# Kernel tuning notes

Hardware: AMD Instinct MI355X
Metric: run time of the kernel (lower is better)

## Reference

```python
import jax, jax.numpy as jnp
import numpy as np

# ---- static config (matches init_kwargs) ----
B, N, D, FH, FW, C = 2, 6, 48, 16, 44, 80
OGH, OGW, DOWNSAMPLE = 256, 704, 16
D_MIN, D_MAX = 2.0, 58.0
XB = (-51.2, 51.2, 0.4); YB = (-51.2, 51.2, 0.4); ZB = (-10.0, 10.0, 20.0)
NX, NY, NZ = 256, 256, 1  # (ub-lb)/step per bound
DX = jnp.array([XB[2], YB[2], ZB[2]], jnp.float32)
LOWER = jnp.array([XB[0], YB[0], ZB[0]], jnp.float32)  # bx - dx/2


def _frustum():
    # UD depth discretization: d_i = d_min + i*(d_max-d_min)/D
    ds = D_MIN + (D_MAX - D_MIN) / D * np.arange(D, dtype=np.float32)
    ds = np.broadcast_to(ds[:, None, None], (D, FH, FW))
    xs = np.broadcast_to(np.linspace(0, OGW - 1, FW, dtype=np.float32)[None, None, :], (D, FH, FW))
    ys = np.broadcast_to(np.linspace(0, OGH - 1, FH, dtype=np.float32)[None, :, None], (D, FH, FW))
    return jnp.asarray(np.stack([xs, ys, ds], -1))  # [D,FH,FW,3]

FRUSTUM = _frustum()


def setup_inputs() -> dict:
    key = jax.random.key(0)
    k1, k2 = jax.random.split(key)
    x = jax.random.normal(k1, (B, N, D, FH, FW, C), dtype=jnp.float32)
    # camera-to-ego rotation: ego_x = z_cam (fwd), ego_y = -x_cam, ego_z = -y_cam
    R = np.array([[0.0, 0.0, 1.0], [-1.0, 0.0, 0.0], [0.0, -1.0, 0.0]], np.float32)
    rots = jnp.asarray(np.broadcast_to(R, (B, N, 3, 3)).copy())
    trans = 2.0 * jax.random.normal(k2, (B, N, 3), dtype=jnp.float32)
    K = np.array([[500.0, 0.0, OGW / 2.0], [0.0, 500.0, OGH / 2.0], [0.0, 0.0, 1.0]], np.float32)
    intrins = jnp.asarray(np.broadcast_to(K, (B, N, 3, 3)).copy())
    post_rots = jnp.asarray(np.broadcast_to(np.eye(3, dtype=np.float32), (B, N, 3, 3)).copy())
    post_trans = jnp.zeros((B, N, 3), jnp.float32)
    return {"x": x, "rots": rots, "trans": trans, "intrins": intrins,
            "post_rots": post_rots, "post_trans": post_trans}


def _get_geometry(rots, trans, intrins, post_rots, post_trans):
    # frustum -> ego-frame 3D points: [B,N,D,FH,FW,3]
    pts = FRUSTUM[None, None] - post_trans[:, :, None, None, None, :]
    inv_post = jnp.linalg.inv(post_rots)
    pts = jnp.einsum('bnij,bndhwj->bndhwi', inv_post, pts)
    # un-normalize pixel coords by depth
    pts = jnp.concatenate([pts[..., :2] * pts[..., 2:3], pts[..., 2:3]], axis=-1)
    combine = jnp.einsum('bnij,bnjk->bnik', rots, jnp.linalg.inv(intrins))
    pts = jnp.einsum('bnij,bndhwj->bndhwi', combine, pts)
    return pts + trans[:, :, None, None, None, :]


def _voxel_pooling(geom, x):
    Nprime = B * N * D * FH * FW
    xf = x.reshape(Nprime, C)
    # voxel indices; torch .long() truncates toward zero -> astype matches
    gi = ((geom.reshape(Nprime, 3) - LOWER) / DX).astype(jnp.int32)
    batch_ix = jnp.repeat(jnp.arange(B, dtype=jnp.int32), Nprime // B)
    kept = ((gi[:, 0] >= 0) & (gi[:, 0] < NX) &
            (gi[:, 1] >= 0) & (gi[:, 1] < NY) &
            (gi[:, 2] >= 0) & (gi[:, 2] < NZ))
    gi = jnp.where(kept[:, None], gi, 0)
    # flat index into (B, NZ, NY, NX); equivalent aggregation to sort+quickcumsum
    flat = ((batch_ix * NZ + gi[:, 2]) * NY + gi[:, 1]) * NX + gi[:, 0]
    xm = jnp.where(kept[:, None], xf, 0.0)
    pooled = jax.ops.segment_sum(xm, flat, num_segments=B * NZ * NY * NX)
    final = pooled.reshape(B, NZ, NY, NX, C).transpose(0, 4, 1, 2, 3)
    return final  # [B, C, NZ, NY, NX]


def reference(x, rots, trans, intrins, post_rots, post_trans):
    geom = _get_geometry(rots, trans, intrins, post_rots, post_trans)
    return _voxel_pooling(geom, x)
```

## Files before the change

kernel.cpp:

```cpp
#include <hip/hip_runtime.h>


#define NCH       80
#define GRID_HW   65536
#define OUT_PER_B 5242880
#define HSTRIDE   3520
#define PTS_PER_BN 33792
#define CAP       32

#define N_ENT_MAX 405504
#define P_BYTES   129761280u
#define NEXT_OFF  129761280u
#define HEAD_OFF  131383296u
#define CNT_OFF   131907584u
#define META_OFF  131907840u
#define WS_NEED   133529856u

__device__ inline void inv3(const double a[9], double inv[9]) {
    double c00 =  a[4]*a[8] - a[5]*a[7];
    double c01 = -(a[3]*a[8] - a[5]*a[6]);
    double c02 =  a[3]*a[7] - a[4]*a[6];
    double det = a[0]*c00 + a[1]*c01 + a[2]*c02;
    double id  = 1.0/det;
    inv[0] = c00*id;
    inv[1] = (a[2]*a[7]-a[1]*a[8])*id;
    inv[2] = (a[1]*a[5]-a[2]*a[4])*id;
    inv[3] = c01*id;
    inv[4] = (a[0]*a[8]-a[2]*a[6])*id;
    inv[5] = (a[2]*a[3]-a[0]*a[5])*id;
    inv[6] = c02*id;
    inv[7] = (a[1]*a[6]-a[0]*a[7])*id;
    inv[8] = (a[0]*a[4]-a[1]*a[3])*id;
}

__device__ inline void prep_bn(const float* __restrict__ rots,
                               const float* __restrict__ trans,
                               const float* __restrict__ intrins,
                               const float* __restrict__ post_rots,
                               const float* __restrict__ post_trans,
                               int bn, double* o) {
    double pr[9], kk[9], rt[9], ipr[9], ik[9];
    #pragma unroll
    for (int i = 0; i < 9; i++) {
        pr[i] = (double)post_rots[bn*9 + i];
        kk[i] = (double)intrins[bn*9 + i];
        rt[i] = (double)rots[bn*9 + i];
    }
    inv3(pr, ipr);
    inv3(kk, ik);
    #pragma unroll
    for (int i = 0; i < 9; i++) o[i] = ipr[i];
    #pragma unroll
    for (int r = 0; r < 3; r++)
        #pragma unroll
        for (int c = 0; c < 3; c++)
            o[9 + r*3 + c] = rt[r*3+0]*ik[0*3+c] + rt[r*3+1]*ik[1*3+c] + rt[r*3+2]*ik[2*3+c];
    #pragma unroll
    for (int i = 0; i < 3; i++) o[18 + i] = (double)post_trans[bn*3 + i];
    #pragma unroll
    for (int i = 0; i < 3; i++) o[21 + i] = (double)trans[bn*3 + i];
}

__global__ void prep_kernel(const float* __restrict__ rots,
                            const float* __restrict__ trans,
                            const float* __restrict__ intrins,
                            const float* __restrict__ post_rots,
                            const float* __restrict__ post_trans,
                            double* __restrict__ tw) {
    int bn = threadIdx.x;
    if (bn >= 12) return;
    prep_bn(rots, trans, intrins, post_rots, post_trans, bn, tw + bn*24);
}

__global__ __launch_bounds__(256) void zero_kernel(float4* __restrict__ p, int n4) {
    int i = blockIdx.x * 256 + threadIdx.x;
    int stride = gridDim.x * 256;
    for (; i < n4; i += stride) p[i] = make_float4(0.f, 0.f, 0.f, 0.f);
}

__global__ __launch_bounds__(256) void init_heads(int* __restrict__ head, int* __restrict__ counter) {
    int i = blockIdx.x * 256 + threadIdx.x;
    if (i < 131072) head[i] = -1;
    if (i == 0) counter[0] = 0;
}

__device__ inline void geom_points(const double* __restrict__ t,
                                   int b, int d, int tid, int* s_base) {
    const float dsv = __fadd_rn(2.0f, __fmul_rn((float)(56.0 / 48.0), (float)d));
    for (int idx = tid; idx < 704; idx += 256) {
        const int h = idx / 44;
        const int w = idx - h * 44;
        float xsv = (w == 43) ? 703.0f : (float)((double)w * (703.0 / 43.0));
        float ysv = (float)(h * 17);
        double px = (double)xsv - t[18];
        double py = (double)ysv - t[19];
        double pz = (double)dsv - t[20];
        double q0 = t[0]*px + t[1]*py + t[2]*pz;
        double q1 = t[3]*px + t[4]*py + t[5]*pz;
        double q2 = t[6]*px + t[7]*py + t[8]*pz;
        q0 *= q2;
        q1 *= q2;
        double e0 = t[9]*q0  + t[10]*q1 + t[11]*q2 + t[21];
        double e1 = t[12]*q0 + t[13]*q1 + t[14]*q2 + t[22];
        double e2 = t[15]*q0 + t[16]*q1 + t[17]*q2 + t[23];
        const double lxy = (double)(-51.2f);
        const double dxy = (double)(0.4f);
        int gx = (int)((e0 - lxy) / dxy);
        int gy = (int)((e1 - lxy) / dxy);
        int gz = (int)((e2 - (double)(-10.0f)) / (double)(20.0f));
        int base = -1;
        if (gx >= 0 && gx < 256 && gy >= 0 && gy < 256 && gz == 0)
            base = (b << 16) | (gy << 8) | gx;
        s_base[idx] = base;
    }
}

__global__ __launch_bounds__(256) void geom_groups(const float* __restrict__ rots,
                                                   const float* __restrict__ trans,
                                                   const float* __restrict__ intrins,
                                                   const float* __restrict__ post_rots,
                                                   const float* __restrict__ post_trans,
                                                   int* __restrict__ nxt,
                                                   int* __restrict__ head,
                                                   int* __restrict__ counter,
                                                   unsigned* __restrict__ ent_meta) {
    __shared__ double   s_t[24];
    __shared__ int      s_base[704];
    __shared__ int      s_gbase[704];
    __shared__ unsigned s_gmask[704];
    __shared__ int      s_gcount[44];
    __shared__ int      s_goff[44];
    __shared__ int      s_eb;

    const int tid   = threadIdx.x;
    const int slice = blockIdx.x;
    const int bn    = slice / 48;
    const int d     = slice - bn * 48;
    const int b     = bn / 6;

    if (tid == 0)
        prep_bn(rots, trans, intrins, post_rots, post_trans, bn, s_t);
    __syncthreads();

    geom_points(s_t, b, d, tid, s_base);
    __syncthreads();

    if (tid < 44) {
        int gb[16]; unsigned gm[16];
        int cnt = 0;
        #pragma unroll
        for (int h = 0; h < 16; h++) {
            int pb = s_base[h * 44 + tid];
            if (pb >= 0) {
                int j = 0;
                for (; j < cnt; j++) if (gb[j] == pb) break;
                if (j < cnt) gm[j] |= (1u << h);
                else { gb[cnt] = pb; gm[cnt] = (1u << h); cnt++; }
            }
        }
        s_gcount[tid] = cnt;
        for (int j = 0; j < cnt; j++) {
            s_gbase[tid * 16 + j] = gb[j];
            s_gmask[tid * 16 + j] = gm[j];
        }
    }
    __syncthreads();

    if (tid == 0) {
        int off = 0;
        for (int w = 0; w < 44; w++) { s_goff[w] = off; off += s_gcount[w]; }
        s_eb = atomicAdd(counter, off);
    }
    __syncthreads();

    if (tid < 44) {
        int off = s_goff[tid];
        int cnt = s_gcount[tid];
        for (int k = 0; k < cnt; k++) {
            int e = s_eb + off + k;
            ent_meta[e] = ((unsigned)slice << 22) | ((unsigned)tid << 16)
                        | (s_gmask[tid * 16 + k] & 0xFFFFu);
            nxt[e] = atomicExch(&head[s_gbase[tid * 16 + k]], e);
        }
    }
}

__global__ __launch_bounds__(256) void reduce_kernel(const float* __restrict__ x,
                                                     const unsigned* __restrict__ ent_meta,
                                                     const int* __restrict__ counter,
                                                     float* __restrict__ P) {
    const int NE = counter[0];
    const int total = NE * 20;
    int i = blockIdx.x * 256 + threadIdx.x;
    const int stride = gridDim.x * 256;
    for (; i < total; i += stride) {
        int e  = i / 20;
        int c4 = i - e * 20;
        unsigned meta = ent_meta[e];
        int slice   = (int)(meta >> 22);
        int w       = (int)((meta >> 16) & 63u);
        unsigned mm = meta & 0xFFFFu;
        const float* xb = x + (size_t)(slice * 704 + w) * NCH + c4 * 4;
        float ax = 0.f, ay = 0.f, az = 0.f, aw = 0.f;
        #pragma unroll
        for (int h = 0; h < 16; h++) {
            float4 v = *(const float4*)(xb + h * HSTRIDE);
            float m = (float)((mm >> h) & 1u);
            ax = fmaf(m, v.x, ax);
            ay = fmaf(m, v.y, ay);
            az = fmaf(m, v.z, az);
            aw = fmaf(m, v.w, aw);
        }
        float4 r; r.x = ax; r.y = ay; r.z = az; r.w = aw;
        *(float4*)(P + (size_t)e * NCH + c4 * 4) = r;
    }
}

__global__ __launch_bounds__(256, 4) void gather_tiled(const float* __restrict__ P,
                                                       const int* __restrict__ nxt,
                                                       const int* __restrict__ head,
                                                       float* __restrict__ out) {
    __shared__ float tile[64 * 81];
    __shared__ int   s_ent[64 * CAP];
    __shared__ int   s_cnt[64];
    __shared__ int   s_ovf[64];

    const int tid = threadIdx.x;
    const int b   = blockIdx.x >> 10;
    const int v0  = (blockIdx.x & 1023) * 64;

    if (tid < 64) {
        int e = head[(b << 16) + v0 + tid];
        int c = 0;
        while (e >= 0 && c < CAP) { s_ent[tid * CAP + c] = e; c++; e = nxt[e]; }
        s_cnt[tid] = c;
        s_ovf[tid] = e;
    }
    __syncthreads();

    #pragma unroll
    for (int i = 0; i < 5; i++) {
        int j  = i * 256 + tid;
        int v  = j / 20;
        int c4 = j - v * 20;
        double dx = 0.0, dy = 0.0, dz = 0.0, dw = 0.0;
        const int cnt = s_cnt[v];
        for (int k = 0; k < cnt; k++) {
            const float4 p = *(const float4*)(P + (size_t)s_ent[v * CAP + k] * NCH + c4 * 4);
            dx += (double)p.x; dy += (double)p.y; dz += (double)p.z; dw += (double)p.w;
        }
        int e = s_ovf[v];
        while (e >= 0) {
            const float4 p = *(const float4*)(P + (size_t)e * NCH + c4 * 4);
            dx += (double)p.x; dy += (double)p.y; dz += (double)p.z; dw += (double)p.w;
            e = nxt[e];
        }
        tile[v * 81 + c4 * 4 + 0] = (float)dx;
        tile[v * 81 + c4 * 4 + 1] = (float)dy;
        tile[v * 81 + c4 * 4 + 2] = (float)dz;
        tile[v * 81 + c4 * 4 + 3] = (float)dw;
    }
    __syncthreads();

    float* dst = out + (size_t)b * OUT_PER_B + v0;
    #pragma unroll
    for (int i = 0; i < 20; i++) {
        int k  = i * 256 + tid;
        int c  = k >> 6;
        int lv = k & 63;
        dst[(size_t)c * GRID_HW + lv] = tile[lv * 81 + c];
    }
}

__global__ __launch_bounds__(256) void scatter_direct_kernel(const float* __restrict__ x,
                                                             const double* __restrict__ ws,
                                                             float* __restrict__ out) {
    __shared__ int      s_base[704];
    __shared__ int      s_colbase[44];
    __shared__ unsigned s_mask[44];
    __shared__ unsigned s_fb[44];

    const int tid = threadIdx.x;
    const int bn  = blockIdx.x / 48;
    const int d   = blockIdx.x - bn * 48;
    const int b   = bn / 6;
    geom_points(ws + bn * 24, b, d, tid, s_base);
    __syncthreads();

    if (tid < 44) {
        int cb = -1; unsigned mm = 0, fb = 0;
        #pragma unroll
        for (int h = 0; h < 16; h++) {
            int pb = s_base[h * 44 + tid];
            if (pb >= 0) {
                if (cb < 0) cb = pb;
                if (pb == cb) mm |= (1u << h);
                else          fb |= (1u << h);
            }
        }
        s_colbase[tid] = cb;
        s_mask[tid]    = mm;
        s_fb[tid]      = fb;
    }
    __syncthreads();

    const float* xb0 = x + ((size_t)bn * PTS_PER_BN + (size_t)d * 704) * NCH;
    #pragma unroll
    for (int pass = 0; pass < 4; pass++) {
        int item = pass * 256 + tid;
        if (item >= 880) break;
        int w  = item / 20;
        int c4 = item - w * 20;
        unsigned mm = s_mask[w];
        unsigned fb = s_fb[w];
        if (!(mm | fb)) continue;
        const float* xb = xb0 + (size_t)w * NCH + c4 * 4;
        float ax = 0.f, ay = 0.f, az = 0.f, aw = 0.f;
        #pragma unroll
        for (int h = 0; h < 16; h++) {
            if ((mm >> h) & 1u) {
                float4 v = *(const float4*)(xb + h * HSTRIDE);
                ax += v.x; ay += v.y; az += v.z; aw += v.w;
            } else if ((fb >> h) & 1u) {
                float4 v = *(const float4*)(xb + h * HSTRIDE);
                int vb = s_base[h * 44 + w];
                float* o = out + (size_t)(vb >> 16) * OUT_PER_B + (vb & 65535);
                atomicAdd(o + (size_t)(c4*4 + 0) * GRID_HW, v.x);
                atomicAdd(o + (size_t)(c4*4 + 1) * GRID_HW, v.y);
                atomicAdd(o + (size_t)(c4*4 + 2) * GRID_HW, v.z);
                atomicAdd(o + (size_t)(c4*4 + 3) * GRID_HW, v.w);
            }
        }
        if (mm) {
            int vb = s_colbase[w];
            float* o = out + (size_t)(vb >> 16) * OUT_PER_B + (vb & 65535);
            atomicAdd(o + (size_t)(c4*4 + 0) * GRID_HW, ax);
            atomicAdd(o + (size_t)(c4*4 + 1) * GRID_HW, ay);
            atomicAdd(o + (size_t)(c4*4 + 2) * GRID_HW, az);
            atomicAdd(o + (size_t)(c4*4 + 3) * GRID_HW, aw);
        }
    }
}

extern "C" void kernel_launch(void* const* d_in, const int* in_sizes, int n_in,
                              void* d_out, int out_size, void* d_ws, size_t ws_size,
                              hipStream_t stream) {
    const float* x          = (const float*)d_in[0];
    const float* rots       = (const float*)d_in[1];
    const float* trans      = (const float*)d_in[2];
    const float* intrins    = (const float*)d_in[3];
    const float* post_rots  = (const float*)d_in[4];
    const float* post_trans = (const float*)d_in[5];
    float* out = (float*)d_out;

    if (ws_size >= (size_t)WS_NEED) {
        float*    P       = (float*)d_ws;
        int*      nxt     = (int*)((char*)d_ws + NEXT_OFF);
        int*      head    = (int*)((char*)d_ws + HEAD_OFF);
        int*      counter = (int*)((char*)d_ws + CNT_OFF);
        unsigned* meta    = (unsigned*)((char*)d_ws + META_OFF);
        init_heads<<<512, 256, 0, stream>>>(head, counter);
        geom_groups<<<576, 256, 0, stream>>>(rots, trans, intrins,
                                             post_rots, post_trans,
                                             nxt, head, counter, meta);
        reduce_kernel<<<2048, 256, 0, stream>>>(x, meta, counter, P);
        gather_tiled<<<2048, 256, 0, stream>>>(P, nxt, head, out);
    } else if (ws_size >= 12 * 24 * sizeof(double)) {
        double* tw = (double*)d_ws;
        zero_kernel<<<2560, 256, 0, stream>>>((float4*)out, out_size / 16);
        prep_kernel<<<1, 64, 0, stream>>>(rots, trans, intrins, post_rots, post_trans, tw);
        scatter_direct_kernel<<<576, 256, 0, stream>>>(x, tw, out);
    }
}
```

Before: 229.9 us.

## Replace per-slice grouping with per-column geometry kernel using wave prefix-scan allocation

Replaces the block-per-slice geometry/grouping kernel with a kernel where each thread handles one image column: it computes 16 voxel ids and groups only consecutive equal voxels. Entry slots are allocated with a wavefront prefix scan and one atomic per wave. The gather switches from double to float accumulation and raises occupancy by halving CAP and allowing 6 blocks per CU. Init and reduce launch sizes also change. Non-adjacent duplicate voxels in a column now become separate entries, and float accumulation can slightly change rounding.

```diff
diff --git a/kernel.cpp b/kernel.cpp
--- a/kernel.cpp
+++ b/kernel.cpp
@@ -6,7 +6,8 @@
 #define OUT_PER_B 5242880
 #define HSTRIDE   3520
 #define PTS_PER_BN 33792
-#define CAP       32
+#define NCOLS     25344
+#define CAP       16
 
 #define N_ENT_MAX 405504
 #define P_BYTES   129761280u
@@ -78,10 +79,198 @@
     for (; i < n4; i += stride) p[i] = make_float4(0.f, 0.f, 0.f, 0.f);
 }
 
-__global__ __launch_bounds__(256) void init_heads(int* __restrict__ head, int* __restrict__ counter) {
+__global__ __launch_bounds__(256) void init_heads(int4* __restrict__ head4, int* __restrict__ counter) {
     int i = blockIdx.x * 256 + threadIdx.x;
-    if (i < 131072) head[i] = -1;
+    head4[i] = make_int4(-1, -1, -1, -1);
     if (i == 0) counter[0] = 0;
+}
+
+__global__ __launch_bounds__(256) void geom_cols(const float* __restrict__ rots,
+                                                 const float* __restrict__ trans,
+                                                 const float* __restrict__ intrins,
+                                                 const float* __restrict__ post_rots,
+                                                 const float* __restrict__ post_trans,
+                                                 int* __restrict__ nxt,
+                                                 int* __restrict__ head,
+                                                 int* __restrict__ counter,
+                                                 unsigned* __restrict__ ent_meta) {
+    __shared__ double s_t[12 * 24];
+
+    const int tid  = threadIdx.x;
+    const int col  = blockIdx.x * 256 + tid;
+    const int lane = tid & 63;
+
+    if (tid < 12)
+        prep_bn(rots, trans, intrins, post_rots, post_trans, tid, s_t + tid * 24);
+    __syncthreads();
+
+    const int slice = col / 44;
+    const int w     = col - slice * 44;
+    const int bn    = slice / 48;
+    const int d     = slice - bn * 48;
+    const int b     = bn / 6;
+    const double* t = s_t + bn * 24;
+
+    int vox[16];
+    {
+        const float dsv = __fadd_rn(2.0f, __fmul_rn((float)(56.0 / 48.0), (float)d));
+        const float xsv = (w == 43) ? 703.0f : (float)((double)w * (703.0 / 43.0));
+        const double px = (double)xsv - t[18];
+        #pragma unroll
+        for (int h = 0; h < 16; h++) {
+            float ysv = (float)(h * 17);
+            double py = (double)ysv - t[19];
+            double pz = (double)dsv - t[20];
+            double q0 = t[0]*px + t[1]*py + t[2]*pz;
+            double q1 = t[3]*px + t[4]*py + t[5]*pz;
+            double q2 = t[6]*px + t[7]*py + t[8]*pz;
+            q0 *= q2;
+            q1 *= q2;
+            double e0 = t[9]*q0  + t[10]*q1 + t[11]*q2 + t[21];
+            double e1 = t[12]*q0 + t[13]*q1 + t[14]*q2 + t[22];
+            double e2 = t[15]*q0 + t[16]*q1 + t[17]*q2 + t[23];
+            const double lxy = (double)(-51.2f);
+            const double dxy = (double)(0.4f);
+            int gx = (int)((e0 - lxy) / dxy);
+            int gy = (int)((e1 - lxy) / dxy);
+            int gz = (int)((e2 - (double)(-10.0f)) / (double)(20.0f));
+            vox[h] = (gx >= 0 && gx < 256 && gy >= 0 && gy < 256 && gz == 0)
+                   ? ((b << 16) | (gy << 8) | gx) : -1;
+        }
+    }
+
+    int cnt = 0;
+    #pragma unroll
+    for (int h = 0; h < 16; h++) {
+        int prev = (h == 0) ? -1 : vox[h - 1];
+        if (vox[h] >= 0 && vox[h] != prev) cnt++;
+    }
+
+    int pre = cnt;
+    #pragma unroll
+    for (int off = 1; off < 64; off <<= 1) {
+        int n = __shfl_up(pre, off);
+        if (lane >= off) pre += n;
+    }
+    int wtot  = __shfl(pre, 63);
+    int wbase = 0;
+    if (wtot > 0) {
+        if (lane == 63) wbase = atomicAdd(counter, wtot);
+        wbase = __shfl(wbase, 63);
+    }
+    int e = wbase + pre - cnt;
+
+    int cur = -1; unsigned mask = 0;
+    #pragma unroll
+    for (int h = 0; h < 16; h++) {
+        if (vox[h] < 0) {
+            if (cur >= 0) {
+                ent_meta[e] = ((unsigned)slice << 22) | ((unsigned)w << 16) | mask;
+                nxt[e] = atomicExch(&head[cur], e);
+                e++; cur = -1; mask = 0;
+            }
+        } else if (vox[h] != cur) {
+            if (cur >= 0) {
+                ent_meta[e] = ((unsigned)slice << 22) | ((unsigned)w << 16) | mask;
+                nxt[e] = atomicExch(&head[cur], e);
+                e++;
+            }
+            cur = vox[h]; mask = (1u << h);
+        } else {
+            mask |= (1u << h);
+        }
+    }
+    if (cur >= 0) {
+        ent_meta[e] = ((unsigned)slice << 22) | ((unsigned)w << 16) | mask;
+        nxt[e] = atomicExch(&head[cur], e);
+    }
+}
+
+__global__ __launch_bounds__(256) void reduce_kernel(const float* __restrict__ x,
+                                                     const unsigned* __restrict__ ent_meta,
+                                                     const int* __restrict__ counter,
+                                                     float* __restrict__ P) {
+    const int NE = counter[0];
+    const int total = NE * 20;
+    int i = blockIdx.x * 256 + threadIdx.x;
+    const int stride = gridDim.x * 256;
+    for (; i < total; i += stride) {
+        int e  = i / 20;
+        int c4 = i - e * 20;
+        unsigned meta = ent_meta[e];
+        int slice   = (int)(meta >> 22);
+        int w       = (int)((meta >> 16) & 63u);
+        unsigned mm = meta & 0xFFFFu;
+        const float* xb = x + (size_t)(slice * 704 + w) * NCH + c4 * 4;
+        float ax = 0.f, ay = 0.f, az = 0.f, aw = 0.f;
+        #pragma unroll
+        for (int h = 0; h < 16; h++) {
+            float4 v = *(const float4*)(xb + h * HSTRIDE);
+            float m = (float)((mm >> h) & 1u);
+            ax = fmaf(m, v.x, ax);
+            ay = fmaf(m, v.y, ay);
+            az = fmaf(m, v.z, az);
+            aw = fmaf(m, v.w, aw);
+        }
+        float4 r; r.x = ax; r.y = ay; r.z = az; r.w = aw;
+        *(float4*)(P + (size_t)e * NCH + c4 * 4) = r;
+    }
+}
+
+__global__ __launch_bounds__(256, 6) void gather_tiled(const float* __restrict__ P,
+                                                       const int* __restrict__ nxt,
+                                                       const int* __restrict__ head,
+                                                       float* __restrict__ out) {
+    __shared__ float tile[64 * 81];
+    __shared__ int   s_ent[64 * CAP];
+    __shared__ int   s_cnt[64];
+    __shared__ int   s_ovf[64];
+
+    const int tid = threadIdx.x;
+    const int b   = blockIdx.x >> 10;
+    const int v0  = (blockIdx.x & 1023) * 64;
+
+    if (tid < 64) {
+        int e = head[(b << 16) + v0 + tid];
+        int c = 0;
+        while (e >= 0 && c < CAP) { s_ent[tid * CAP + c] = e; c++; e = nxt[e]; }
+        s_cnt[tid] = c;
+        s_ovf[tid] = e;
+    }
+    __syncthreads();
+
+    #pragma unroll
+    for (int i = 0; i < 5; i++) {
+        int j  = i * 256 + tid;
+        int v  = j / 20;
+        int c4 = j - v * 20;
+        float ax = 0.f, ay = 0.f, az = 0.f, aw = 0.f;
+        const int cnt = s_cnt[v];
+        for (int k = 0; k < cnt; k++) {
+            const float4 p = *(const float4*)(P + (size_t)s_ent[v * CAP + k] * NCH + c4 * 4);
+            ax += p.x; ay += p.y; az += p.z; aw += p.w;
+        }
+        int e = s_ovf[v];
+        while (e >= 0) {
+            const float4 p = *(const float4*)(P + (size_t)e * NCH + c4 * 4);
+            ax += p.x; ay += p.y; az += p.z; aw += p.w;
+            e = nxt[e];
+        }
+        tile[v * 81 + c4 * 4 + 0] = ax;
+        tile[v * 81 + c4 * 4 + 1] = ay;
+        tile[v * 81 + c4 * 4 + 2] = az;
+        tile[v * 81 + c4 * 4 + 3] = aw;
+    }
+    __syncthreads();
+
+    float* dst = out + (size_t)b * OUT_PER_B + v0;
+    #pragma unroll
+    for (int i = 0; i < 20; i++) {
+        int k  = i * 256 + tid;
+        int c  = k >> 6;
+        int lv = k & 63;
+        dst[(size_t)c * GRID_HW + lv] = tile[lv * 81 + c];
+    }
 }
 
 __device__ inline void geom_points(const double* __restrict__ t,
@@ -115,163 +304,6 @@
     }
 }
 
-__global__ __launch_bounds__(256) void geom_groups(const float* __restrict__ rots,
-                                                   const float* __restrict__ trans,
-                                                   const float* __restrict__ intrins,
-                                                   const float* __restrict__ post_rots,
-                                                   const float* __restrict__ post_trans,
-                                                   int* __restrict__ nxt,
-                                                   int* __restrict__ head,
-                                                   int* __restrict__ counter,
-                                                   unsigned* __restrict__ ent_meta) {
-    __shared__ double   s_t[24];
-    __shared__ int      s_base[704];
-    __shared__ int      s_gbase[704];
-    __shared__ unsigned s_gmask[704];
-    __shared__ int      s_gcount[44];
-    __shared__ int      s_goff[44];
-    __shared__ int      s_eb;
-
-    const int tid   = threadIdx.x;
-    const int slice = blockIdx.x;
-    const int bn    = slice / 48;
-    const int d     = slice - bn * 48;
-    const int b     = bn / 6;
-
-    if (tid == 0)
-        prep_bn(rots, trans, intrins, post_rots, post_trans, bn, s_t);
-    __syncthreads();
-
-    geom_points(s_t, b, d, tid, s_base);
-    __syncthreads();
-
-    if (tid < 44) {
-        int gb[16]; unsigned gm[16];
-        int cnt = 0;
-        #pragma unroll
-        for (int h = 0; h < 16; h++) {
-            int pb = s_base[h * 44 + tid];
-            if (pb >= 0) {
-                int j = 0;
-                for (; j < cnt; j++) if (gb[j] == pb) break;
-                if (j < cnt) gm[j] |= (1u << h);
-                else { gb[cnt] = pb; gm[cnt] = (1u << h); cnt++; }
-            }
-        }
-        s_gcount[tid] = cnt;
-        for (int j = 0; j < cnt; j++) {
-            s_gbase[tid * 16 + j] = gb[j];
-            s_gmask[tid * 16 + j] = gm[j];
-        }
-    }
-    __syncthreads();
-
-    if (tid == 0) {
-        int off = 0;
-        for (int w = 0; w < 44; w++) { s_goff[w] = off; off += s_gcount[w]; }
-        s_eb = atomicAdd(counter, off);
-    }
-    __syncthreads();
-
-    if (tid < 44) {
-        int off = s_goff[tid];
-        int cnt = s_gcount[tid];
-        for (int k = 0; k < cnt; k++) {
-            int e = s_eb + off + k;
-            ent_meta[e] = ((unsigned)slice << 22) | ((unsigned)tid << 16)
-                        | (s_gmask[tid * 16 + k] & 0xFFFFu);
-            nxt[e] = atomicExch(&head[s_gbase[tid * 16 + k]], e);
-        }
-    }
-}
-
-__global__ __launch_bounds__(256) void reduce_kernel(const float* __restrict__ x,
-                                                     const unsigned* __restrict__ ent_meta,
-                                                     const int* __restrict__ counter,
-                                                     float* __restrict__ P) {
-    const int NE = counter[0];
-    const int total = NE * 20;
-    int i = blockIdx.x * 256 + threadIdx.x;
-    const int stride = gridDim.x * 256;
-    for (; i < total; i += stride) {
-        int e  = i / 20;
-        int c4 = i - e * 20;
-        unsigned meta = ent_meta[e];
-        int slice   = (int)(meta >> 22);
-        int w       = (int)((meta >> 16) & 63u);
-        unsigned mm = meta & 0xFFFFu;
-        const float* xb = x + (size_t)(slice * 704 + w) * NCH + c4 * 4;
-        float ax = 0.f, ay = 0.f, az = 0.f, aw = 0.f;
-        #pragma unroll
-        for (int h = 0; h < 16; h++) {
-            float4 v = *(const float4*)(xb + h * HSTRIDE);
-            float m = (float)((mm >> h) & 1u);
-            ax = fmaf(m, v.x, ax);
-            ay = fmaf(m, v.y, ay);
-            az = fmaf(m, v.z, az);
-            aw = fmaf(m, v.w, aw);
-        }
-        float4 r; r.x = ax; r.y = ay; r.z = az; r.w = aw;
-        *(float4*)(P + (size_t)e * NCH + c4 * 4) = r;
-    }
-}
-
-__global__ __launch_bounds__(256, 4) void gather_tiled(const float* __restrict__ P,
-                                                       const int* __restrict__ nxt,
-                                                       const int* __restrict__ head,
-                                                       float* __restrict__ out) {
-    __shared__ float tile[64 * 81];
-    __shared__ int   s_ent[64 * CAP];
-    __shared__ int   s_cnt[64];
-    __shared__ int   s_ovf[64];
-
-    const int tid = threadIdx.x;
-    const int b   = blockIdx.x >> 10;
-    const int v0  = (blockIdx.x & 1023) * 64;
-
-    if (tid < 64) {
-        int e = head[(b << 16) + v0 + tid];
-        int c = 0;
-        while (e >= 0 && c < CAP) { s_ent[tid * CAP + c] = e; c++; e = nxt[e]; }
-        s_cnt[tid] = c;
-        s_ovf[tid] = e;
-    }
-    __syncthreads();
-
-    #pragma unroll
-    for (int i = 0; i < 5; i++) {
-        int j  = i * 256 + tid;
-        int v  = j / 20;
-        int c4 = j - v * 20;
-        double dx = 0.0, dy = 0.0, dz = 0.0, dw = 0.0;
-        const int cnt = s_cnt[v];
-        for (int k = 0; k < cnt; k++) {
-            const float4 p = *(const float4*)(P + (size_t)s_ent[v * CAP + k] * NCH + c4 * 4);
-            dx += (double)p.x; dy += (double)p.y; dz += (double)p.z; dw += (double)p.w;
-        }
-        int e = s_ovf[v];
-        while (e >= 0) {
-            const float4 p = *(const float4*)(P + (size_t)e * NCH + c4 * 4);
-            dx += (double)p.x; dy += (double)p.y; dz += (double)p.z; dw += (double)p.w;
-            e = nxt[e];
-        }
-        tile[v * 81 + c4 * 4 + 0] = (float)dx;
-        tile[v * 81 + c4 * 4 + 1] = (float)dy;
-        tile[v * 81 + c4 * 4 + 2] = (float)dz;
-        tile[v * 81 + c4 * 4 + 3] = (float)dw;
-    }
-    __syncthreads();
-
-    float* dst = out + (size_t)b * OUT_PER_B + v0;
-    #pragma unroll
-    for (int i = 0; i < 20; i++) {
-        int k  = i * 256 + tid;
-        int c  = k >> 6;
-        int lv = k & 63;
-        dst[(size_t)c * GRID_HW + lv] = tile[lv * 81 + c];
-    }
-}
-
 __global__ __launch_bounds__(256) void scatter_direct_kernel(const float* __restrict__ x,
                                                              const double* __restrict__ ws,
                                                              float* __restrict__ out) {
@@ -359,11 +391,11 @@
         int*      head    = (int*)((char*)d_ws + HEAD_OFF);
         int*      counter = (int*)((char*)d_ws + CNT_OFF);
         unsigned* meta    = (unsigned*)((char*)d_ws + META_OFF);
-        init_heads<<<512, 256, 0, stream>>>(head, counter);
-        geom_groups<<<576, 256, 0, stream>>>(rots, trans, intrins,
-                                             post_rots, post_trans,
-                                             nxt, head, counter, meta);
-        reduce_kernel<<<2048, 256, 0, stream>>>(x, meta, counter, P);
+        init_heads<<<128, 256, 0, stream>>>((int4*)head, counter);
+        geom_cols<<<99, 256, 0, stream>>>(rots, trans, intrins,
+                                          post_rots, post_trans,
+                                          nxt, head, counter, meta);
+        reduce_kernel<<<1024, 256, 0, stream>>>(x, meta, counter, P);
         gather_tiled<<<2048, 256, 0, stream>>>(P, nxt, head, out);
     } else if (ws_size >= 12 * 24 * sizeof(double)) {
         double* tw = (double*)d_ws;
```

New measurement: 224.8 us. -2.2%, faster.
